# Kernel tuning notes

Hardware: AMD Instinct MI355X
Metric: run time of the kernel (lower is better)

## Reference

```python
import jax, jax.numpy as jnp
import numpy as np

B, N, C = 8, 2000, 512
H, W, SR = 8, 5, 2          # num_heads, window_size, sr_ratio
LN_EPS = 1e-5


def setup_inputs() -> dict:
    key = jax.random.key(0)
    ks = jax.random.split(key, 6)
    s = lambda k, shape: jax.random.normal(k, shape, jnp.float32) * 0.02
    return {
        "x": jax.random.normal(ks[0], (B, N, C), jnp.float32),
        "Wq": s(ks[1], (C, C)),      "bq": jnp.zeros((C,), jnp.float32),
        "Wkv": s(ks[2], (2 * C, C)), "bkv": jnp.zeros((2 * C,), jnp.float32),
        "Wc": s(ks[3], (C, C)),      "bc": jnp.zeros((C,), jnp.float32),
        "ln_g": jnp.ones((C,), jnp.float32), "ln_b": jnp.zeros((C,), jnp.float32),
        "Wp": s(ks[4], (C, C)),      "bp": jnp.zeros((C,), jnp.float32),
    }


def reference(x, Wq, bq, Wkv, bkv, Wc, bc, ln_g, ln_b, Wp, bp):
    Bx, Nx, Cx = x.shape
    hd = Cx // H
    scale = hd ** (-0.5)
    G = Nx // W          # number of local windows
    M = Nx // SR         # pooled length

    # q: [B,H,N,hd]
    q = (x @ Wq.T + bq).reshape(Bx, Nx, H, hd).transpose(0, 2, 1, 3)

    # local kv: [B,G,W,2,H,hd] -> k_l/v_l [B,H,G,W,hd]
    kv = (x @ Wkv.T + bkv).reshape(Bx, G, W, 2, H, hd)
    k_l = kv[:, :, :, 0].transpose(0, 3, 1, 2, 4)
    v_l = kv[:, :, :, 1].transpose(0, 3, 1, 2, 4)

    # windowed local scores: group q into windows, einsum within window
    # (equivalent to torch's repeat_interleave + per-query matmul, but no blowup)
    qw = q.reshape(Bx, H, G, W, hd)
    attn_local = jnp.einsum('bhgqd,bhgkd->bhgqk', qw, k_l).reshape(Bx, H, Nx, W) * scale

    # pooled branch: AvgPool1d(sr) -> 1x1 conv -> LayerNorm -> GELU(exact)
    xp = x.reshape(Bx, M, SR, Cx).mean(axis=2)
    xp = xp @ Wc.T + bc
    mu = xp.mean(-1, keepdims=True)
    var = xp.var(-1, keepdims=True)
    xp = (xp - mu) / jnp.sqrt(var + LN_EPS) * ln_g + ln_b
    xp = jax.nn.gelu(xp, approximate=False)

    kvp = (xp @ Wkv.T + bkv).reshape(Bx, M, 2, H, hd)
    k_p = kvp[:, :, 0].transpose(0, 2, 1, 3)   # [B,H,M,hd]
    v_p = kvp[:, :, 1].transpose(0, 2, 1, 3)

    attn_pool = jnp.einsum('bhnd,bhmd->bhnm', q, k_p) * scale  # [B,H,N,M]

    # joint softmax over local window + pooled keys
    attn = jax.nn.softmax(jnp.concatenate([attn_local, attn_pool], axis=-1), axis=-1)
    a_l = attn[..., :W].reshape(Bx, H, G, W, W)
    a_p = attn[..., W:]

    x_l = jnp.einsum('bhgqk,bhgkd->bhgqd', a_l, v_l).reshape(Bx, H, Nx, hd)
    x_p = jnp.einsum('bhnm,bhmd->bhnd', a_p, v_p)

    out = (x_l + x_p).transpose(0, 2, 1, 3).reshape(Bx, Nx, Cx)
    return out @ Wp.T + bp
```

## Files before the change

kernel.cpp:

```cpp
#include <hip/hip_runtime.h>
#include <hip/hip_bf16.h>
#include <math.h>

#define B_   8
#define N_   2000
#define C_   512
#define H_   8
#define W_   5
#define SR_  2
#define M_   1000
#define HD_  64
#define KK_  512
#define RP_  8192
#define NPAD_ 16384
#define LN_EPS_ 1e-5f
#define SCALE_  0.125f
#define QSC_    0.18033688011112042f

#define TQ_   128
#define NCH_  16
#define KSTR2 72

typedef __attribute__((ext_vector_type(8))) short bf16x8;
typedef __attribute__((ext_vector_type(4))) short short4v;
typedef __attribute__((ext_vector_type(4))) float f32x4;
typedef __attribute__((ext_vector_type(16))) float f32x16;
#define MFMA16(a,b,c) __builtin_amdgcn_mfma_f32_16x16x32_bf16(a,b,c,0,0,0)
#define MFMA32(a,b,c) __builtin_amdgcn_mfma_f32_32x32x16_bf16(a,b,c,0,0,0)

__device__ __forceinline__ short f2bf(float f) {
  unsigned u = __float_as_uint(f);
  u += 0x7FFFu + ((u >> 16) & 1u);
  return (short)(u >> 16);
}
__device__ __forceinline__ uint2 pack4bf(float4 v) {
  unsigned a = ((unsigned)(unsigned short)f2bf(v.x)) | (((unsigned)(unsigned short)f2bf(v.y)) << 16);
  unsigned b = ((unsigned)(unsigned short)f2bf(v.z)) | (((unsigned)(unsigned short)f2bf(v.w)) << 16);
  return make_uint2(a, b);
}

__device__ __forceinline__ float wave_sum(float v) {
#pragma unroll
  for (int o = 32; o > 0; o >>= 1) v += __shfl_xor(v, o);
  return v;
}

__device__ __forceinline__ void gl_lds16(const void* g, void* l) {
  __builtin_amdgcn_global_load_lds(
      (const __attribute__((address_space(1))) void*)g,
      (__attribute__((address_space(3))) void*)l, 16, 0, 0);
}

__global__ __launch_bounds__(256) void cvt_bf16(const float* __restrict__ src,
                                                short* __restrict__ dst, int n8) {
  int i = blockIdx.x * 256 + threadIdx.x;
  if (i >= n8) return;
  float4 a = reinterpret_cast<const float4*>(src)[i * 2];
  float4 b = reinterpret_cast<const float4*>(src)[i * 2 + 1];
  uint2 pa = pack4bf(a), pb = pack4bf(b);
  reinterpret_cast<uint4*>(dst)[i] = make_uint4(pa.x, pa.y, pb.x, pb.y);
}

__global__ __launch_bounds__(256) void cvt_pool(const float* __restrict__ X,
                                                short* __restrict__ Xb,
                                                short* __restrict__ Xp) {
  int idx = blockIdx.x * 256 + threadIdx.x;
  const int total = B_ * M_ * (C_ / 8);
  if (idx >= total) return;
  int row = idx / (C_ / 8);
  int c8  = idx % (C_ / 8);
  int b = row / M_, m = row % M_;
  size_t r0 = ((size_t)b * N_ + 2 * m) * C_ + c8 * 8;
  size_t r1 = r0 + C_;
  float4 a0 = *(const float4*)(X + r0), a1 = *(const float4*)(X + r0 + 4);
  float4 b0 = *(const float4*)(X + r1), b1 = *(const float4*)(X + r1 + 4);
  uint2 pa0 = pack4bf(a0), pa1 = pack4bf(a1);
  uint2 pb0 = pack4bf(b0), pb1 = pack4bf(b1);
  *(uint4*)(Xb + r0) = make_uint4(pa0.x, pa0.y, pa1.x, pa1.y);
  *(uint4*)(Xb + r1) = make_uint4(pb0.x, pb0.y, pb1.x, pb1.y);
  float4 s0, s1;
  s0.x = 0.5f * (a0.x + b0.x); s0.y = 0.5f * (a0.y + b0.y);
  s0.z = 0.5f * (a0.z + b0.z); s0.w = 0.5f * (a0.w + b0.w);
  s1.x = 0.5f * (a1.x + b1.x); s1.y = 0.5f * (a1.y + b1.y);
  s1.z = 0.5f * (a1.z + b1.z); s1.w = 0.5f * (a1.w + b1.w);
  uint2 q0 = pack4bf(s0), q1 = pack4bf(s1);
  *(uint4*)(Xp + (size_t)row * C_ + c8 * 8) = make_uint4(q0.x, q0.y, q1.x, q1.y);
}

template<int OUT_BF16>
__global__ __launch_bounds__(256) void gemm_mfma(const short* __restrict__ A,
                                                 const short* __restrict__ Bm,
                                                 const float* __restrict__ bias,
                                                 void* __restrict__ Yv,
                                                 int O, float oscale) {
  __shared__ short As[128 * 32];
  __shared__ short Bs[128 * 32];
  const int tid  = threadIdx.x;
  const int w    = tid >> 6;
  const int lane = tid & 63;
  const int g    = lane >> 4;
  const int c0   = lane & 15;
  const int wr   = w >> 1;
  const int wc   = w & 1;
  const long r0 = (long)blockIdx.y * 128;
  const long o0 = (long)blockIdx.x * 128;
  const int srow = lane >> 2;
  const int scol = (lane & 3) * 8;

  f32x4 acc[4][4];
#pragma unroll
  for (int m = 0; m < 4; ++m)
#pragma unroll
    for (int n = 0; n < 4; ++n) acc[m][n] = (f32x4){0.f, 0.f, 0.f, 0.f};

  for (int kk = 0; kk < 16; ++kk) {
    __syncthreads();
#pragma unroll
    for (int i = 0; i < 2; ++i) {
      int arow = i * 64 + w * 16;
      gl_lds16(A  + (r0 + arow + srow) * KK_ + kk * 32 + scol, &As[arow * 32]);
      gl_lds16(Bm + (o0 + arow + srow) * KK_ + kk * 32 + scol, &Bs[arow * 32]);
    }
    __syncthreads();
    bf16x8 a[4], b[4];
#pragma unroll
    for (int m = 0; m < 4; ++m) a[m] = *(const bf16x8*)&As[(wr * 64 + m * 16 + c0) * 32 + g * 8];
#pragma unroll
    for (int n = 0; n < 4; ++n) b[n] = *(const bf16x8*)&Bs[(wc * 64 + n * 16 + c0) * 32 + g * 8];
#pragma unroll
    for (int m = 0; m < 4; ++m)
#pragma unroll
      for (int n = 0; n < 4; ++n) acc[m][n] = MFMA16(a[m], b[n], acc[m][n]);
  }

#pragma unroll
  for (int m = 0; m < 4; ++m) {
    long row = r0 + wr * 64 + m * 16 + g * 4;
#pragma unroll
    for (int n = 0; n < 4; ++n) {
      long col = o0 + wc * 64 + n * 16 + c0;
      float bv = bias[col];
#pragma unroll
      for (int r = 0; r < 4; ++r) {
        float v = (acc[m][n][r] + bv) * oscale;
        if (OUT_BF16) ((short*)Yv)[(row + r) * O + col] = f2bf(v);
        else          ((float*)Yv)[(row + r) * O + col] = v;
      }
    }
  }
}

__global__ __launch_bounds__(256) void gemm_qkv(const short* __restrict__ A,
                                                const short* __restrict__ Bm,
                                                const float* __restrict__ bq,
                                                const float* __restrict__ bkv,
                                                short* __restrict__ Yq,
                                                short* __restrict__ Ykv) {
  __shared__ short As[128 * 32];
  __shared__ short Bs[128 * 32];
  const int tid  = threadIdx.x;
  const int w    = tid >> 6;
  const int lane = tid & 63;
  const int g    = lane >> 4;
  const int c0   = lane & 15;
  const int wr   = w >> 1;
  const int wc   = w & 1;
  const long r0 = (long)blockIdx.y * 128;
  const long o0 = (long)blockIdx.x * 128;
  const int srow = lane >> 2;
  const int scol = (lane & 3) * 8;

  f32x4 acc[4][4];
#pragma unroll
  for (int m = 0; m < 4; ++m)
#pragma unroll
    for (int n = 0; n < 4; ++n) acc[m][n] = (f32x4){0.f, 0.f, 0.f, 0.f};

  for (int kk = 0; kk < 16; ++kk) {
    __syncthreads();
#pragma unroll
    for (int i = 0; i < 2; ++i) {
      int arow = i * 64 + w * 16;
      gl_lds16(A  + (r0 + arow + srow) * KK_ + kk * 32 + scol, &As[arow * 32]);
      gl_lds16(Bm + (o0 + arow + srow) * KK_ + kk * 32 + scol, &Bs[arow * 32]);
    }
    __syncthreads();
    bf16x8 a[4], b[4];
#pragma unroll
    for (int m = 0; m < 4; ++m) a[m] = *(const bf16x8*)&As[(wr * 64 + m * 16 + c0) * 32 + g * 8];
#pragma unroll
    for (int n = 0; n < 4; ++n) b[n] = *(const bf16x8*)&Bs[(wc * 64 + n * 16 + c0) * 32 + g * 8];
#pragma unroll
    for (int m = 0; m < 4; ++m)
#pragma unroll
      for (int n = 0; n < 4; ++n) acc[m][n] = MFMA16(a[m], b[n], acc[m][n]);
  }

  const bool isq = (blockIdx.x < 4);
#pragma unroll
  for (int m = 0; m < 4; ++m) {
    long row = r0 + wr * 64 + m * 16 + g * 4;
#pragma unroll
    for (int n = 0; n < 4; ++n) {
      long col = o0 + wc * 64 + n * 16 + c0;
      if (isq) {
        float bv = bq[col];
#pragma unroll
        for (int r = 0; r < 4; ++r)
          Yq[(row + r) * 512 + col] = f2bf((acc[m][n][r] + bv) * QSC_);
      } else {
        long ck = col - 512;
        float bv = bkv[ck];
#pragma unroll
        for (int r = 0; r < 4; ++r)
          Ykv[(row + r) * 1024 + ck] = f2bf(acc[m][n][r] + bv);
      }
    }
  }
}

__global__ __launch_bounds__(256) void ln_gelu(const float* __restrict__ Xc,
                                               short* __restrict__ Xo,
                                               const float* __restrict__ gam,
                                               const float* __restrict__ bet) {
  const int row = blockIdx.x;
  const float* p = Xc + (size_t)row * C_;
  const int t = threadIdx.x;
  float v0 = p[t], v1 = p[t + 256];
  float s  = wave_sum(v0 + v1);
  float ss = wave_sum(v0 * v0 + v1 * v1);
  __shared__ float rs[4], rss[4];
  const int w = t >> 6, lane = t & 63;
  if (lane == 0) { rs[w] = s; rss[w] = ss; }
  __syncthreads();
  float ts  = rs[0] + rs[1] + rs[2] + rs[3];
  float tss = rss[0] + rss[1] + rss[2] + rss[3];
  float mean = ts * (1.0f / C_);
  float var  = tss * (1.0f / C_) - mean * mean;
  float rstd = rsqrtf(var + LN_EPS_);
  float u0 = (v0 - mean) * rstd * gam[t]       + bet[t];
  float u1 = (v1 - mean) * rstd * gam[t + 256] + bet[t + 256];
  Xo[(size_t)row * C_ + t]       = f2bf(u0 * 0.5f * (1.0f + erff(u0 * 0.70710678118654752f)));
  Xo[(size_t)row * C_ + t + 256] = f2bf(u1 * 0.5f * (1.0f + erff(u1 * 0.70710678118654752f)));
}

template<int MODE>
__device__ __forceinline__ void tile32(const short* Ksb, const short* Vtb,
                                       const bf16x8 qf[4],
                                       float& l_c, f32x16* o,
                                       int c, int hi, int koff)
{
  f32x16 sblk[2];
  __builtin_amdgcn_s_setprio(1);
#pragma unroll
  for (int kb = 0; kb < 2; ++kb) {
    f32x16 acc = {};
#pragma unroll
    for (int sl = 0; sl < 4; ++sl) {
      bf16x8 kf = *(const bf16x8*)&Ksb[(kb*32 + c)*KSTR2 + sl*16 + hi*8];
      acc = MFMA32(kf, qf[sl], acc);
    }
    sblk[kb] = acc;
  }
  __builtin_amdgcn_s_setprio(0);

  if (MODE == 1) {
#pragma unroll
    for (int kb = 0; kb < 2; ++kb)
#pragma unroll
      for (int r = 0; r < 16; ++r) {
        int ku = koff + kb*32 + ((r & 3) + 8*(r >> 2));
        if ((unsigned)ku >= 5u) sblk[kb][r] = -3.0e38f;
      }
  }
  if (MODE == 2) {
#pragma unroll
    for (int r = 4; r < 16; ++r) sblk[1][r] = -3.0e38f;
  }

  float rs4[4] = {0.f, 0.f, 0.f, 0.f};
  int dw[2][8];
#pragma unroll
  for (int kb = 0; kb < 2; ++kb)
#pragma unroll
    for (int i = 0; i < 8; ++i) {
      float p0 = exp2f(sblk[kb][2*i]);
      float p1 = exp2f(sblk[kb][2*i + 1]);
      rs4[i & 3] += p0 + p1;
      int d;
      asm("v_cvt_pk_bf16_f32 %0, %1, %2" : "=v"(d) : "v"(p0), "v"(p1));
      dw[kb][i] = d;
    }
  float rs = (rs4[0] + rs4[1]) + (rs4[2] + rs4[3]);
  rs += __shfl_xor(rs, 32);
  l_c += rs;

  bf16x8 pfrag[2][2];
#pragma unroll
  for (int kb = 0; kb < 2; ++kb)
#pragma unroll
    for (int kp = 0; kp < 2; ++kp) {
      union { int i[4]; bf16x8 v; } u;
      u.i[0] = dw[kb][kp*4 + 0];
      u.i[1] = dw[kb][kp*4 + 1];
      u.i[2] = dw[kb][kp*4 + 2];
      u.i[3] = dw[kb][kp*4 + 3];
      pfrag[kb][kp] = u.v;
    }

  __builtin_amdgcn_s_setprio(1);
#pragma unroll
  for (int db = 0; db < 2; ++db)
#pragma unroll
    for (int kb = 0; kb < 2; ++kb)
#pragma unroll
      for (int kp = 0; kp < 2; ++kp) {
        bf16x8 vf = *(const bf16x8*)&Vtb[(db*32 + c)*KSTR2 + kb*32 + kp*16 + hi*8];
        o[db] = MFMA32(vf, pfrag[kb][kp], o[db]);
      }
  __builtin_amdgcn_s_setprio(0);
}

__global__ __launch_bounds__(256, 4) void attn_mfma32(const short* __restrict__ Q,
                                                      const short* __restrict__ KV,
                                                      const short* __restrict__ KVP,
                                                      short* __restrict__ Oa) {
  __shared__ __align__(16) short Ks[2][64 * KSTR2];
  __shared__ __align__(16) short Vt[2][64 * KSTR2];

  const int bid   = blockIdx.x;
  const int bh    = bid & 63;
  const int chunk = bid >> 6;
  const int b     = bh >> 3;
  const int h     = bh & 7;
  const int n0    = chunk * TQ_;
  const int tid  = threadIdx.x;
  const int wq   = tid >> 6;
  const int lane = tid & 63;
  const int c    = lane & 31;
  const int hi   = lane >> 5;

  const int qabs = n0 + wq * 32 + c;
  const size_t qrow = (size_t)(b * N_ + qabs) * C_ + h * HD_;
  bf16x8 qf[4];
#pragma unroll
  for (int sl = 0; sl < 4; ++sl) qf[sl] = *(const bf16x8*)(Q + qrow + sl*16 + hi*8);

  const int qlo = (qabs / 5) * 5;
  const int klo = (n0 / 5) * 5;
  const int wlo = ((n0 + wq*32) / 5) * 5;
  const int whi = ((n0 + wq*32 + 31) / 5) * 5 + 5;

  const int kkey = tid >> 3, kdq = tid & 7;
  const int vkp  = tid & 31, vdq = (tid >> 5) & 7;
  const int svkp = (vkp & ~6) | ((vkp & 2) << 1) | ((vkp & 4) >> 1);
  bf16x8 rk0, rk1, rv0, rv1;

  auto issue = [&](const short* pb_) {
    rk0 = *(const bf16x8*)(pb_ + (size_t)kkey        * (2*C_) + h*HD_ + kdq*8);
    rk1 = *(const bf16x8*)(pb_ + (size_t)(kkey + 32) * (2*C_) + h*HD_ + kdq*8);
    rv0 = *(const bf16x8*)(pb_ + (size_t)(2*vkp)     * (2*C_) + C_ + h*HD_ + vdq*8);
    rv1 = *(const bf16x8*)(pb_ + (size_t)(2*vkp + 1) * (2*C_) + C_ + h*HD_ + vdq*8);
  };
  auto write = [&](int buf) {
    *(bf16x8*)&Ks[buf][kkey * KSTR2 + kdq * 8]        = rk0;
    *(bf16x8*)&Ks[buf][(kkey + 32) * KSTR2 + kdq * 8] = rk1;
#pragma unroll
    for (int e = 0; e < 8; ++e) {
      unsigned wv = ((unsigned)(unsigned short)rv0[e]) | (((unsigned)(unsigned short)rv1[e]) << 16);
      *(unsigned*)&Vt[buf][(vdq*8 + e) * KSTR2 + 2*svkp] = wv;
    }
  };

  const short* kvloc = KV  + (size_t)(b * N_ + klo) * (2*C_);
  const short* kvp_b = KVP + (size_t)(b * M_)       * (2*C_);

  float l_c = 0.f;
  f32x16 o[2];
  o[0] = (f32x16){}; o[1] = (f32x16){};

  issue(kvloc);
  write(0);
  __syncthreads();
  int cur = 0;

#pragma unroll 1
  for (int t = 0; t < 3; ++t) {
    const short* nxt = (t < 2) ? kvloc + (size_t)(t + 1) * 64 * (2*C_) : kvp_b;
    issue(nxt);
    const int base = klo + t * 64;
    if (base < whi && base + 64 > wlo)
      tile32<1>(Ks[cur], Vt[cur], qf, l_c, o, c, hi, base + 4*hi - qlo);
    write(cur ^ 1);
    __syncthreads();
    cur ^= 1;
  }
#pragma unroll 1
  for (int t = 0; t < 15; ++t) {
    issue(kvp_b + (size_t)(t + 1) * 64 * (2*C_));
    tile32<0>(Ks[cur], Vt[cur], qf, l_c, o, c, hi, 0);
    write(cur ^ 1);
    __syncthreads();
    cur ^= 1;
  }
  tile32<2>(Ks[cur], Vt[cur], qf, l_c, o, c, hi, 0);

  if (qabs < N_) {
    float inv = 1.0f / l_c;
    short* orow = Oa + ((size_t)(b * N_ + qabs)) * C_ + h * HD_;
#pragma unroll
    for (int db = 0; db < 2; ++db)
#pragma unroll
      for (int rq = 0; rq < 4; ++rq) {
        short4v sv;
#pragma unroll
        for (int i = 0; i < 4; ++i) sv[i] = f2bf(o[db][rq*4 + i] * inv);
        *(short4v*)(orow + db*32 + rq*8 + 4*hi) = sv;
      }
  }
}

extern "C" void kernel_launch(void* const* d_in, const int* in_sizes, int n_in,
                              void* d_out, int out_size, void* d_ws, size_t ws_size,
                              hipStream_t stream) {
  const float* x   = (const float*)d_in[0];
  const float* Wq  = (const float*)d_in[1];
  const float* bq  = (const float*)d_in[2];
  const float* Wkv = (const float*)d_in[3];
  const float* bkv = (const float*)d_in[4];
  const float* Wc  = (const float*)d_in[5];
  const float* bc  = (const float*)d_in[6];
  const float* lng = (const float*)d_in[7];
  const float* lnb = (const float*)d_in[8];
  const float* Wp  = (const float*)d_in[9];
  const float* bp  = (const float*)d_in[10];
  float* out = (float*)d_out;

  float* xc   = (float*)d_ws;
  short* sb   = (short*)(xc + (size_t)RP_ * 512);
  short* xb    = sb;
  short* qb    = xb   + (size_t)16000 * 512;
  short* kvb   = qb   + (size_t)NPAD_ * 512;
  short* xpb   = kvb  + (size_t)NPAD_ * 1024;
  short* xcb   = xpb  + (size_t)RP_ * 512;
  short* kvpb  = xcb  + (size_t)RP_ * 512;
  short* aoutb = kvpb + (size_t)RP_ * 1024;
  short* Wqkvb = aoutb + (size_t)16000 * 512;
  short* Wcb   = Wqkvb + (size_t)1536 * 512;
  short* Wpb   = Wcb  + (size_t)512 * 512;

  dim3 blk(256);

  cvt_pool<<<dim3((B_*M_*(C_/8) + 255)/256), blk, 0, stream>>>(x, xb, xpb);
  cvt_bf16<<<dim3((512*512/8  + 255)/256), blk, 0, stream>>>(Wq,  Wqkvb,             512*512/8);
  cvt_bf16<<<dim3((1024*512/8 + 255)/256), blk, 0, stream>>>(Wkv, Wqkvb + 512*512,   1024*512/8);
  cvt_bf16<<<dim3((512*512/8  + 255)/256), blk, 0, stream>>>(Wc,  Wcb,  512*512/8);
  cvt_bf16<<<dim3((512*512/8  + 255)/256), blk, 0, stream>>>(Wp,  Wpb,  512*512/8);

  gemm_mfma<0><<<dim3(C_/128, RP_/128), blk, 0, stream>>>(xpb, Wcb, bc, xc, C_, 1.0f);
  ln_gelu<<<dim3(B_ * M_), blk, 0, stream>>>(xc, xcb, lng, lnb);
  gemm_mfma<1><<<dim3((2*C_)/128, RP_/128), blk, 0, stream>>>(xcb, Wqkvb + 512*512, bkv, kvpb, 2*C_, 1.0f);

  gemm_qkv<<<dim3(1536/128, 16000/128), blk, 0, stream>>>(xb, Wqkvb, bq, bkv, qb, kvb);

  attn_mfma32<<<dim3(64 * NCH_), blk, 0, stream>>>(qb, kvb, kvpb, aoutb);

  gemm_mfma<0><<<dim3(C_/128, 16000/128), blk, 0, stream>>>(aoutb, Wpb, bp, out, C_, 1.0f);
}
```

Baseline: 188.3 us.

## Double attention query tile to 256 with 512-thread blocks sharing K/V loads

The attention kernel now handles 256 queries per block using 8 waves instead of 128 queries with 4 waves. This halves the number of blocks that each stream the full pooled K/V for a given batch and head, which cuts global and L2 traffic per query. The K and V tile loads are split so that one half of the threads fetches K and the other half fetches and transposes V. The local-window loop grows from 3 to 5 tiles to cover the wider query span. The trade-offs are half as many blocks in the grid and heavier register and LDS pressure per CU from the larger blocks.

Measured after the change: 184.0 us. -2.3%, faster.

```diff
diff --git a/kernel.cpp b/kernel.cpp
--- a/kernel.cpp
+++ b/kernel.cpp
@@ -17,8 +17,9 @@
 #define SCALE_  0.125f
 #define QSC_    0.18033688011112042f
 
-#define TQ_   128
-#define NCH_  16
+#define TQ_   256
+#define NCH_  8
+#define LT_   5
 #define KSTR2 72
 
 typedef __attribute__((ext_vector_type(8))) short bf16x8;
@@ -321,7 +322,7 @@
   __builtin_amdgcn_s_setprio(0);
 }
 
-__global__ __launch_bounds__(256, 4) void attn_mfma32(const short* __restrict__ Q,
+__global__ __launch_bounds__(512, 4) void attn_mfma32(const short* __restrict__ Q,
                                                       const short* __restrict__ KV,
                                                       const short* __restrict__ KVP,
                                                       short* __restrict__ Oa) {
@@ -351,24 +352,32 @@
   const int wlo = ((n0 + wq*32) / 5) * 5;
   const int whi = ((n0 + wq*32 + 31) / 5) * 5 + 5;
 
-  const int kkey = tid >> 3, kdq = tid & 7;
-  const int vkp  = tid & 31, vdq = (tid >> 5) & 7;
+  const bool isK = (tid < 256);
+  const int u    = tid & 255;
+  const int kkey = u >> 3, kdq = u & 7;
+  const int vkp  = u & 31, vdq = (u >> 5) & 7;
   const int svkp = (vkp & ~6) | ((vkp & 2) << 1) | ((vkp & 4) >> 1);
-  bf16x8 rk0, rk1, rv0, rv1;
+  bf16x8 r0v, r1v;
 
   auto issue = [&](const short* pb_) {
-    rk0 = *(const bf16x8*)(pb_ + (size_t)kkey        * (2*C_) + h*HD_ + kdq*8);
-    rk1 = *(const bf16x8*)(pb_ + (size_t)(kkey + 32) * (2*C_) + h*HD_ + kdq*8);
-    rv0 = *(const bf16x8*)(pb_ + (size_t)(2*vkp)     * (2*C_) + C_ + h*HD_ + vdq*8);
-    rv1 = *(const bf16x8*)(pb_ + (size_t)(2*vkp + 1) * (2*C_) + C_ + h*HD_ + vdq*8);
+    if (isK) {
+      r0v = *(const bf16x8*)(pb_ + (size_t)kkey        * (2*C_) + h*HD_ + kdq*8);
+      r1v = *(const bf16x8*)(pb_ + (size_t)(kkey + 32) * (2*C_) + h*HD_ + kdq*8);
+    } else {
+      r0v = *(const bf16x8*)(pb_ + (size_t)(2*vkp)     * (2*C_) + C_ + h*HD_ + vdq*8);
+      r1v = *(const bf16x8*)(pb_ + (size_t)(2*vkp + 1) * (2*C_) + C_ + h*HD_ + vdq*8);
+    }
   };
   auto write = [&](int buf) {
-    *(bf16x8*)&Ks[buf][kkey * KSTR2 + kdq * 8]        = rk0;
-    *(bf16x8*)&Ks[buf][(kkey + 32) * KSTR2 + kdq * 8] = rk1;
-#pragma unroll
-    for (int e = 0; e < 8; ++e) {
-      unsigned wv = ((unsigned)(unsigned short)rv0[e]) | (((unsigned)(unsigned short)rv1[e]) << 16);
-      *(unsigned*)&Vt[buf][(vdq*8 + e) * KSTR2 + 2*svkp] = wv;
+    if (isK) {
+      *(bf16x8*)&Ks[buf][kkey * KSTR2 + kdq * 8]        = r0v;
+      *(bf16x8*)&Ks[buf][(kkey + 32) * KSTR2 + kdq * 8] = r1v;
+    } else {
+#pragma unroll
+      for (int e = 0; e < 8; ++e) {
+        unsigned wv = ((unsigned)(unsigned short)r0v[e]) | (((unsigned)(unsigned short)r1v[e]) << 16);
+        *(unsigned*)&Vt[buf][(vdq*8 + e) * KSTR2 + 2*svkp] = wv;
+      }
     }
   };
 
@@ -385,8 +394,8 @@
   int cur = 0;
 
 #pragma unroll 1
-  for (int t = 0; t < 3; ++t) {
-    const short* nxt = (t < 2) ? kvloc + (size_t)(t + 1) * 64 * (2*C_) : kvp_b;
+  for (int t = 0; t < LT_; ++t) {
+    const short* nxt = (t < LT_ - 1) ? kvloc + (size_t)(t + 1) * 64 * (2*C_) : kvp_b;
     issue(nxt);
     const int base = klo + t * 64;
     if (base < whi && base + 64 > wlo)
@@ -463,7 +472,7 @@
 
   gemm_qkv<<<dim3(1536/128, 16000/128), blk, 0, stream>>>(xb, Wqkvb, bq, bkv, qb, kvb);
 
-  attn_mfma32<<<dim3(64 * NCH_), blk, 0, stream>>>(qb, kvb, kvpb, aoutb);
+  attn_mfma32<<<dim3(64 * NCH_), dim3(512), 0, stream>>>(qb, kvb, kvpb, aoutb);
 
   gemm_mfma<0><<<dim3(C_/128, 16000/128), blk, 0, stream>>>(aoutb, Wpb, bp, out, C_, 1.0f);
 }
```
